# Kernel tuning notes

Measured on AMD Instinct MI355X. Metric: run time of the kernel, lower is better.

The kernel has to match this reference:

```python
import jax, jax.numpy as jnp
import numpy as np

D_MODEL = 512
NHEAD = 8
D_K = D_MODEL // NHEAD


def setup_inputs() -> dict:
    key = jax.random.key(0)
    ks = jax.random.split(key, 7)
    B, L = 4, 2048
    x = jax.random.normal(ks[0], (B, L, D_MODEL), dtype=jnp.float32)
    scale = 1.0 / np.sqrt(D_MODEL)
    Wq = jax.random.normal(ks[1], (D_MODEL, D_MODEL), dtype=jnp.float32) * scale
    Wk = jax.random.normal(ks[2], (D_MODEL, D_MODEL), dtype=jnp.float32) * scale
    Wv = jax.random.normal(ks[3], (D_MODEL, D_MODEL), dtype=jnp.float32) * scale
    Wo = jax.random.normal(ks[4], (D_MODEL, D_MODEL), dtype=jnp.float32) * scale
    wave_freq = jax.random.normal(ks[5], (NHEAD,), dtype=jnp.float32) * 0.1
    wave_phase = jnp.zeros((NHEAD,), dtype=jnp.float32)
    return {"x": x, "Wq": Wq, "Wk": Wk, "Wv": Wv, "Wo": Wo,
            "wave_freq": wave_freq, "wave_phase": wave_phase}


def reference(x, Wq, Wk, Wv, Wo, wave_freq, wave_phase):
    B, L, D = x.shape
    H, dk = NHEAD, D_K
    # nn.Linear(bias=False): y = x @ W.T
    q = (x @ Wq.T).reshape(B, L, H, dk).transpose(0, 2, 1, 3)  # (B,H,L,dk)
    k = (x @ Wk.T).reshape(B, L, H, dk).transpose(0, 2, 1, 3)
    v = (x @ Wv.T).reshape(B, L, H, dk).transpose(0, 2, 1, 3)
    pos = jnp.arange(L, dtype=x.dtype)  # (L,)
    two_pi = jnp.asarray(2.0 * np.pi, dtype=x.dtype)
    # wave: (H, L) -> broadcast as (1, H, 1, L) over key positions
    wave = jnp.cos(two_pi * wave_freq[:, None] * pos[None, :] + wave_phase[:, None])
    scores = jnp.einsum('bhqd,bhkd->bhqk', q, k) * (dk ** -0.5)
    scores = scores * wave[None, :, None, :]
    attn = jax.nn.softmax(scores, axis=-1)
    out = jnp.einsum('bhqk,bhkd->bhqd', attn, v)
    out = out.transpose(0, 2, 1, 3).reshape(B, L, D)
    return out @ Wo.T
```

## Files before the change

kernel.cpp:

```cpp
#include <hip/hip_runtime.h>
#include <math.h>

#define D_MODEL 512
#define NHEAD   8
#define DK      64
#define BATCH   4
#define SEQ     2048
#define MTOT    (BATCH*SEQ)
#define NXELEM  (MTOT*D_MODEL)
#define NWELEM  (4*D_MODEL*D_MODEL)

typedef _Float16 half8   __attribute__((ext_vector_type(8)));
typedef _Float16 half4_t __attribute__((ext_vector_type(4)));
typedef float    f32x4   __attribute__((ext_vector_type(4)));

#define MFMA32(a,b,c) __builtin_amdgcn_mfma_f32_16x16x32_f16((a),(b),(c),0,0,0)

__global__ __launch_bounds__(256) void cvt_kernel(
    const float* __restrict__ x,
    const float* __restrict__ Wq, const float* __restrict__ Wk,
    const float* __restrict__ Wv, const float* __restrict__ Wo,
    const float* __restrict__ wf, const float* __restrict__ wp,
    _Float16* __restrict__ Xh, _Float16* __restrict__ Wh,
    float* __restrict__ wtab)
{
    const int tid = blockIdx.x * 256 + threadIdx.x;
    int idx = tid * 4;
    if (idx < NXELEM + NWELEM) {
        const float* src; _Float16* dst; int off;
        if (idx < NXELEM) { src = x; dst = Xh; off = idx; }
        else {
            int r = idx - NXELEM;
            int sel = r >> 18;
            off = r & ((1 << 18) - 1);
            src = (sel == 0) ? Wq : (sel == 1) ? Wk : (sel == 2) ? Wv : Wo;
            dst = Wh + ((size_t)sel << 18);
        }
        float4 v = *(const float4*)(src + off);
        half4_t h;
        h[0] = (_Float16)v.x; h[1] = (_Float16)v.y;
        h[2] = (_Float16)v.z; h[3] = (_Float16)v.w;
        *(half4_t*)(dst + off) = h;
    } else {
        int widx = idx - (NXELEM + NWELEM);
        const int h = widx >> 11;
        const int pos0 = widx & 2047;
        const float f  = 6.28318530717958647692f * wf[h];
        const float ph = wp[h];
        float4 o;
        o.x = 0.125f * cosf(fmaf(f, (float)(pos0 + 0), ph));
        o.y = 0.125f * cosf(fmaf(f, (float)(pos0 + 1), ph));
        o.z = 0.125f * cosf(fmaf(f, (float)(pos0 + 2), ph));
        o.w = 0.125f * cosf(fmaf(f, (float)(pos0 + 3), ph));
        *(float4*)(wtab + widx) = o;
    }
}

__global__ __launch_bounds__(256) void qkv_mfma_kernel(
    const _Float16* __restrict__ Xh, const _Float16* __restrict__ Wh,
    const float* __restrict__ wtab,
    _Float16* __restrict__ Qh, _Float16* __restrict__ Kh,
    _Float16* __restrict__ Vth)
{
    __shared__ _Float16 As[128][72];
    __shared__ _Float16 Bs[64][72];

    const int t  = threadIdx.x;
    const int n0 = blockIdx.x * 64;
    const int m0 = blockIdx.y * 128;
    const int which = n0 >> 9;
    const int h = (n0 >> 6) & 7;
    const _Float16* Wbase = Wh + ((size_t)which << 18) + (size_t)(h * 64) * 512;

    const int w = t >> 6, lane = t & 63, ln = lane & 15, quad = lane >> 4;
    const int ar = t >> 1, ac = (t & 1) * 32;
    const int br = t >> 2, bc = (t & 3) * 16;

    const _Float16* ag = Xh + (size_t)(m0 + ar) * 512 + ac;
    const _Float16* bg = Wbase + (size_t)br * 512 + bc;

    const f32x4 kZero = {0.f, 0.f, 0.f, 0.f};
    f32x4 acc[2][4];
    #pragma unroll
    for (int i = 0; i < 2; ++i)
        #pragma unroll
        for (int j = 0; j < 4; ++j) acc[i][j] = kZero;

    for (int k0 = 0; k0 < 512; k0 += 64) {
        half8 av[4], bv[2];
        #pragma unroll
        for (int i = 0; i < 4; ++i) av[i] = *(const half8*)(ag + k0 + i * 8);
        #pragma unroll
        for (int i = 0; i < 2; ++i) bv[i] = *(const half8*)(bg + k0 + i * 8);
        __syncthreads();
        #pragma unroll
        for (int i = 0; i < 4; ++i) *(half8*)&As[ar][ac + i * 8] = av[i];
        #pragma unroll
        for (int i = 0; i < 2; ++i) *(half8*)&Bs[br][bc + i * 8] = bv[i];
        __syncthreads();

        #pragma unroll
        for (int ks = 0; ks < 2; ++ks) {
            half8 af[2], bf[4];
            #pragma unroll
            for (int mt = 0; mt < 2; ++mt)
                af[mt] = *(const half8*)&As[w * 32 + mt * 16 + ln][ks * 32 + quad * 8];
            #pragma unroll
            for (int nt = 0; nt < 4; ++nt)
                bf[nt] = *(const half8*)&Bs[nt * 16 + ln][ks * 32 + quad * 8];
            #pragma unroll
            for (int mt = 0; mt < 2; ++mt)
                #pragma unroll
                for (int nt = 0; nt < 4; ++nt)
                    acc[mt][nt] = MFMA32(af[mt], bf[nt], acc[mt][nt]);
        }
    }

    const int b  = m0 >> 11;
    const int l0 = m0 & 2047;

    if (which < 2) {
        _Float16* dst = (which == 0 ? Qh : Kh) + (size_t)(b * NHEAD + h) * SEQ * DK;
        const float* wt = wtab + h * SEQ;
        #pragma unroll
        for (int mt = 0; mt < 2; ++mt)
            #pragma unroll
            for (int r = 0; r < 4; ++r) {
                const int lq = l0 + w * 32 + mt * 16 + quad * 4 + r;
                const float wv = (which == 1) ? wt[lq] : 1.0f;
                #pragma unroll
                for (int nt = 0; nt < 4; ++nt) {
                    const int d = nt * 16 + ln;
                    dst[(size_t)lq * DK + d] = (_Float16)(acc[mt][nt][r] * wv);
                }
            }
    } else {
        __syncthreads();
        _Float16* Vl = &As[0][0];
        #pragma unroll
        for (int mt = 0; mt < 2; ++mt)
            #pragma unroll
            for (int nt = 0; nt < 4; ++nt)
                #pragma unroll
                for (int r = 0; r < 4; ++r) {
                    const int lq = w * 32 + mt * 16 + quad * 4 + r;
                    const int k32 = lq & 31;
                    const int pos = (lq & ~31) | (((k32 >> 2) & 3) << 3)
                                  | ((k32 >> 4) << 2) | (k32 & 3);
                    const int d  = nt * 16 + ln;
                    Vl[d * 136 + pos] = (_Float16)acc[mt][nt][r];
                }
        __syncthreads();
        _Float16* dst = Vth + (size_t)(b * NHEAD + h) * DK * SEQ;
        const int d = t >> 2, c0 = (t & 3) * 32;
        #pragma unroll
        for (int i = 0; i < 4; ++i) {
            half8 v = *(const half8*)&Vl[d * 136 + c0 + i * 8];
            *(half8*)(dst + (size_t)d * SEQ + l0 + c0 + i * 8) = v;
        }
    }
}

__global__ __launch_bounds__(256) void attn_mfma_kernel(
    const _Float16* __restrict__ Qh, const _Float16* __restrict__ Kwh,
    const _Float16* __restrict__ Vth, _Float16* __restrict__ AOh)
{
    __shared__ _Float16 Qs[64][72];
    __shared__ _Float16 Ks[64][72];
    __shared__ _Float16 Vs[64][72];

    const int bh = blockIdx.x;
    const int q0 = blockIdx.y * 64;
    const int b = bh >> 3, h = bh & 7;

    const int t = threadIdx.x;
    const int w = t >> 6, lane = t & 63, ln = lane & 15, quad = lane >> 4;

    const _Float16* Qg = Qh + ((size_t)bh * SEQ + q0) * DK;
    const _Float16* Kg = Kwh + (size_t)bh * SEQ * DK;
    const _Float16* Vg = Vth + (size_t)bh * DK * SEQ;

    const int sr = t >> 2, sc = (t & 3) * 16;

    *(half8*)&Qs[sr][sc]     = *(const half8*)(Qg + (size_t)sr * DK + sc);
    *(half8*)&Qs[sr][sc + 8] = *(const half8*)(Qg + (size_t)sr * DK + sc + 8);
    __syncthreads();
    half8 qf0 = *(const half8*)&Qs[w * 16 + ln][quad * 8];
    half8 qf1 = *(const half8*)&Qs[w * 16 + ln][32 + quad * 8];

    const f32x4 kZero = {0.f, 0.f, 0.f, 0.f};
    f32x4 o[4];
    #pragma unroll
    for (int nt = 0; nt < 4; ++nt) o[nt] = kZero;
    float l_acc = 0.f;

    for (int kt = 0; kt < SEQ; kt += 64) {
        half8 kv0 = *(const half8*)(Kg + (size_t)(kt + sr) * DK + sc);
        half8 kv1 = *(const half8*)(Kg + (size_t)(kt + sr) * DK + sc + 8);
        half8 vv0 = *(const half8*)(Vg + (size_t)sr * SEQ + kt + sc);
        half8 vv1 = *(const half8*)(Vg + (size_t)sr * SEQ + kt + sc + 8);
        __syncthreads();
        *(half8*)&Ks[sr][sc]     = kv0;
        *(half8*)&Ks[sr][sc + 8] = kv1;
        *(half8*)&Vs[sr][sc]     = vv0;
        *(half8*)&Vs[sr][sc + 8] = vv1;
        __syncthreads();

        #pragma unroll
        for (int g = 0; g < 2; ++g) {
            half8 ka0 = *(const half8*)&Ks[(2*g+0) * 16 + ln][quad * 8];
            half8 ka1 = *(const half8*)&Ks[(2*g+0) * 16 + ln][32 + quad * 8];
            half8 kb0 = *(const half8*)&Ks[(2*g+1) * 16 + ln][quad * 8];
            half8 kb1 = *(const half8*)&Ks[(2*g+1) * 16 + ln][32 + quad * 8];
            f32x4 s0 = MFMA32(ka0, qf0, kZero);
            f32x4 s1 = MFMA32(kb0, qf0, kZero);
            s0 = MFMA32(ka1, qf1, s0);
            s1 = MFMA32(kb1, qf1, s1);

            half8 pf;
            float ps = 0.f;
            #pragma unroll
            for (int r = 0; r < 4; ++r) {
                const float e0 = __expf(s0[r]);
                const float e1 = __expf(s1[r]);
                pf[r]     = (_Float16)e0;
                pf[r + 4] = (_Float16)e1;
                ps += e0 + e1;
            }
            l_acc += ps;

            #pragma unroll
            for (int nt = 0; nt < 4; ++nt) {
                half8 vf = *(const half8*)&Vs[nt * 16 + ln][g * 32 + quad * 8];
                o[nt] = MFMA32(pf, vf, o[nt]);
            }
        }
    }

    l_acc += __shfl_xor(l_acc, 16);
    l_acc += __shfl_xor(l_acc, 32);

    #pragma unroll
    for (int r = 0; r < 4; ++r) {
        const float lr  = __shfl(l_acc, quad * 4 + r, 16);
        const float inv = 1.0f / lr;
        const int lq = q0 + w * 16 + quad * 4 + r;
        const size_t base = ((size_t)b * SEQ + lq) * D_MODEL + h * DK;
        #pragma unroll
        for (int nt = 0; nt < 4; ++nt)
            AOh[base + nt * 16 + ln] = (_Float16)(o[nt][r] * inv);
    }
}

__global__ __launch_bounds__(256) void out_mfma_kernel(
    const _Float16* __restrict__ AOh, const _Float16* __restrict__ Woh,
    float* __restrict__ out)
{
    __shared__ _Float16 As[128][72];
    __shared__ _Float16 Bs[64][72];

    const int t  = threadIdx.x;
    const int n0 = blockIdx.x * 64;
    const int m0 = blockIdx.y * 128;

    const int w = t >> 6, lane = t & 63, ln = lane & 15, quad = lane >> 4;
    const int ar = t >> 1, ac = (t & 1) * 32;
    const int br = t >> 2, bc = (t & 3) * 16;

    const _Float16* ag = AOh + (size_t)(m0 + ar) * 512 + ac;
    const _Float16* bg = Woh + (size_t)(n0 + br) * 512 + bc;

    const f32x4 kZero = {0.f, 0.f, 0.f, 0.f};
    f32x4 acc[2][4];
    #pragma unroll
    for (int i = 0; i < 2; ++i)
        #pragma unroll
        for (int j = 0; j < 4; ++j) acc[i][j] = kZero;

    for (int k0 = 0; k0 < 512; k0 += 64) {
        half8 av[4], bv[2];
        #pragma unroll
        for (int i = 0; i < 4; ++i) av[i] = *(const half8*)(ag + k0 + i * 8);
        #pragma unroll
        for (int i = 0; i < 2; ++i) bv[i] = *(const half8*)(bg + k0 + i * 8);
        __syncthreads();
        #pragma unroll
        for (int i = 0; i < 4; ++i) *(half8*)&As[ar][ac + i * 8] = av[i];
        #pragma unroll
        for (int i = 0; i < 2; ++i) *(half8*)&Bs[br][bc + i * 8] = bv[i];
        __syncthreads();

        #pragma unroll
        for (int ks = 0; ks < 2; ++ks) {
            half8 af[2], bf[4];
            #pragma unroll
            for (int mt = 0; mt < 2; ++mt)
                af[mt] = *(const half8*)&As[w * 32 + mt * 16 + ln][ks * 32 + quad * 8];
            #pragma unroll
            for (int nt = 0; nt < 4; ++nt)
                bf[nt] = *(const half8*)&Bs[nt * 16 + ln][ks * 32 + quad * 8];
            #pragma unroll
            for (int mt = 0; mt < 2; ++mt)
                #pragma unroll
                for (int nt = 0; nt < 4; ++nt)
                    acc[mt][nt] = MFMA32(af[mt], bf[nt], acc[mt][nt]);
        }
    }

    #pragma unroll
    for (int mt = 0; mt < 2; ++mt)
        #pragma unroll
        for (int nt = 0; nt < 4; ++nt)
            #pragma unroll
            for (int r = 0; r < 4; ++r) {
                const int gm = m0 + w * 32 + mt * 16 + quad * 4 + r;
                out[(size_t)gm * 512 + n0 + nt * 16 + ln] = acc[mt][nt][r];
            }
}

extern "C" void kernel_launch(void* const* d_in, const int* in_sizes, int n_in,
                              void* d_out, int out_size, void* d_ws, size_t ws_size,
                              hipStream_t stream)
{
    (void)in_sizes; (void)n_in; (void)out_size; (void)ws_size;
    const float* x  = (const float*)d_in[0];
    const float* Wq = (const float*)d_in[1];
    const float* Wk = (const float*)d_in[2];
    const float* Wv = (const float*)d_in[3];
    const float* Wo = (const float*)d_in[4];
    const float* wf = (const float*)d_in[5];
    const float* wp = (const float*)d_in[6];
    float* out = (float*)d_out;

    const size_t NX = (size_t)MTOT * D_MODEL;
    _Float16* Xh  = (_Float16*)d_ws;
    _Float16* Wh  = Xh + NX;
    _Float16* Qh  = Wh + 4 * 262144;
    _Float16* Kh  = Qh + NX;
    _Float16* Vth = Kh + NX;
    _Float16* AOh = Vth + NX;
    float*    wtab = (float*)(AOh + NX);

    cvt_kernel<<<5136, 256, 0, stream>>>(x, Wq, Wk, Wv, Wo, wf, wp, Xh, Wh, wtab);

    dim3 g1(24, 64);
    qkv_mfma_kernel<<<g1, 256, 0, stream>>>(Xh, Wh, wtab, Qh, Kh, Vth);

    dim3 g2(BATCH * NHEAD, SEQ / 64);
    attn_mfma_kernel<<<g2, 256, 0, stream>>>(Qh, Kh, Vth, AOh);

    dim3 g3(8, 64);
    out_mfma_kernel<<<g3, 256, 0, stream>>>(AOh, Wh + 3 * 262144, out);
}
```

Measured before the change: 178.4 us.

## Double-buffer K/V tiles and process 128 queries per attention block

The attention kernel now covers 128 query rows per block, with two 16-row query tiles per wave, so each K/V tile loaded into shared memory is reused twice as often. K/V tiles are double-buffered and the next tile's global loads are issued before the current tile's compute. The grid is flattened to 512 blocks, with an index remap intended to place heads that share K/V close together. The cost is more accumulator registers and half as many blocks, which may lower occupancy and parallelism.

```diff
diff --git a/kernel.cpp b/kernel.cpp
--- a/kernel.cpp
+++ b/kernel.cpp
@@ -165,12 +165,13 @@
     const _Float16* __restrict__ Qh, const _Float16* __restrict__ Kwh,
     const _Float16* __restrict__ Vth, _Float16* __restrict__ AOh)
 {
-    __shared__ _Float16 Qs[64][72];
-    __shared__ _Float16 Ks[64][72];
-    __shared__ _Float16 Vs[64][72];
-
-    const int bh = blockIdx.x;
-    const int q0 = blockIdx.y * 64;
+    __shared__ _Float16 SM[4][64][72];
+
+    const int bx = blockIdx.x;
+    const int g8 = bx & 7;
+    const int s  = bx >> 3;
+    const int bh = g8 * 4 + (s >> 4);
+    const int q0 = (s & 15) * 128;
     const int b = bh >> 3, h = bh & 7;
 
     const int t = threadIdx.x;
@@ -181,75 +182,133 @@
     const _Float16* Vg = Vth + (size_t)bh * DK * SEQ;
 
     const int sr = t >> 2, sc = (t & 3) * 16;
-
-    *(half8*)&Qs[sr][sc]     = *(const half8*)(Qg + (size_t)sr * DK + sc);
-    *(half8*)&Qs[sr][sc + 8] = *(const half8*)(Qg + (size_t)sr * DK + sc + 8);
+    const int qr = t >> 1, qc = (t & 1) * 32;
+
+    {
+        const _Float16* qp = Qg + (size_t)qr * DK + qc;
+        half8 qv0 = *(const half8*)(qp);
+        half8 qv1 = *(const half8*)(qp + 8);
+        half8 qv2 = *(const half8*)(qp + 16);
+        half8 qv3 = *(const half8*)(qp + 24);
+        const _Float16* kp = Kg + (size_t)sr * DK + sc;
+        const _Float16* vp = Vg + (size_t)sr * SEQ + sc;
+        half8 kv0 = *(const half8*)(kp);
+        half8 kv1 = *(const half8*)(kp + 8);
+        half8 vv0 = *(const half8*)(vp);
+        half8 vv1 = *(const half8*)(vp + 8);
+        _Float16* qd = &SM[2 + (qr >> 6)][qr & 63][qc];
+        *(half8*)(qd)      = qv0;
+        *(half8*)(qd + 8)  = qv1;
+        *(half8*)(qd + 16) = qv2;
+        *(half8*)(qd + 24) = qv3;
+        *(half8*)&SM[0][sr][sc]     = kv0;
+        *(half8*)&SM[0][sr][sc + 8] = kv1;
+        *(half8*)&SM[1][sr][sc]     = vv0;
+        *(half8*)&SM[1][sr][sc + 8] = vv1;
+    }
     __syncthreads();
-    half8 qf0 = *(const half8*)&Qs[w * 16 + ln][quad * 8];
-    half8 qf1 = *(const half8*)&Qs[w * 16 + ln][32 + quad * 8];
+
+    half8 qf[2][2];
+    #pragma unroll
+    for (int u = 0; u < 2; ++u) {
+        const int row = w * 32 + u * 16 + ln;
+        const _Float16* qsrc = &SM[2 + (row >> 6)][row & 63][0];
+        qf[u][0] = *(const half8*)(qsrc + quad * 8);
+        qf[u][1] = *(const half8*)(qsrc + 32 + quad * 8);
+    }
+    __syncthreads();
 
     const f32x4 kZero = {0.f, 0.f, 0.f, 0.f};
-    f32x4 o[4];
-    #pragma unroll
-    for (int nt = 0; nt < 4; ++nt) o[nt] = kZero;
-    float l_acc = 0.f;
-
-    for (int kt = 0; kt < SEQ; kt += 64) {
-        half8 kv0 = *(const half8*)(Kg + (size_t)(kt + sr) * DK + sc);
-        half8 kv1 = *(const half8*)(Kg + (size_t)(kt + sr) * DK + sc + 8);
-        half8 vv0 = *(const half8*)(Vg + (size_t)sr * SEQ + kt + sc);
-        half8 vv1 = *(const half8*)(Vg + (size_t)sr * SEQ + kt + sc + 8);
-        __syncthreads();
-        *(half8*)&Ks[sr][sc]     = kv0;
-        *(half8*)&Ks[sr][sc + 8] = kv1;
-        *(half8*)&Vs[sr][sc]     = vv0;
-        *(half8*)&Vs[sr][sc + 8] = vv1;
-        __syncthreads();
+    f32x4 o[2][4];
+    #pragma unroll
+    for (int u = 0; u < 2; ++u)
+        #pragma unroll
+        for (int nt = 0; nt < 4; ++nt) o[u][nt] = kZero;
+    float l_acc[2] = {0.f, 0.f};
+
+    for (int kt = 0; kt < SEQ / 64; ++kt) {
+        const int cur = kt & 1;
+
+        half8 pk0, pk1, pv0, pv1;
+        const bool more = (kt + 1 < SEQ / 64);
+        if (more) {
+            const _Float16* kp = Kg + (size_t)((kt + 1) * 64 + sr) * DK + sc;
+            const _Float16* vp = Vg + (size_t)sr * SEQ + (kt + 1) * 64 + sc;
+            pk0 = *(const half8*)(kp);
+            pk1 = *(const half8*)(kp + 8);
+            pv0 = *(const half8*)(vp);
+            pv1 = *(const half8*)(vp + 8);
+        }
+
+        const _Float16 (*Ks)[72] = SM[2 * cur];
+        const _Float16 (*Vs)[72] = SM[2 * cur + 1];
 
         #pragma unroll
         for (int g = 0; g < 2; ++g) {
-            half8 ka0 = *(const half8*)&Ks[(2*g+0) * 16 + ln][quad * 8];
-            half8 ka1 = *(const half8*)&Ks[(2*g+0) * 16 + ln][32 + quad * 8];
-            half8 kb0 = *(const half8*)&Ks[(2*g+1) * 16 + ln][quad * 8];
-            half8 kb1 = *(const half8*)&Ks[(2*g+1) * 16 + ln][32 + quad * 8];
-            f32x4 s0 = MFMA32(ka0, qf0, kZero);
-            f32x4 s1 = MFMA32(kb0, qf0, kZero);
-            s0 = MFMA32(ka1, qf1, s0);
-            s1 = MFMA32(kb1, qf1, s1);
-
-            half8 pf;
-            float ps = 0.f;
-            #pragma unroll
-            for (int r = 0; r < 4; ++r) {
-                const float e0 = __expf(s0[r]);
-                const float e1 = __expf(s1[r]);
-                pf[r]     = (_Float16)e0;
-                pf[r + 4] = (_Float16)e1;
-                ps += e0 + e1;
+            half8 ka0 = *(const half8*)&Ks[(2 * g + 0) * 16 + ln][quad * 8];
+            half8 ka1 = *(const half8*)&Ks[(2 * g + 0) * 16 + ln][32 + quad * 8];
+            half8 kb0 = *(const half8*)&Ks[(2 * g + 1) * 16 + ln][quad * 8];
+            half8 kb1 = *(const half8*)&Ks[(2 * g + 1) * 16 + ln][32 + quad * 8];
+            half8 vf[4];
+            #pragma unroll
+            for (int nt = 0; nt < 4; ++nt)
+                vf[nt] = *(const half8*)&Vs[nt * 16 + ln][g * 32 + quad * 8];
+
+            #pragma unroll
+            for (int u = 0; u < 2; ++u) {
+                f32x4 s0 = MFMA32(ka0, qf[u][0], kZero);
+                f32x4 s1 = MFMA32(kb0, qf[u][0], kZero);
+                s0 = MFMA32(ka1, qf[u][1], s0);
+                s1 = MFMA32(kb1, qf[u][1], s1);
+
+                half8 pf;
+                float ps = 0.f;
+                #pragma unroll
+                for (int r = 0; r < 4; ++r) {
+                    const float e0 = __expf(s0[r]);
+                    const float e1 = __expf(s1[r]);
+                    pf[r]     = (_Float16)e0;
+                    pf[r + 4] = (_Float16)e1;
+                    ps += e0 + e1;
+                }
+                l_acc[u] += ps;
+
+                #pragma unroll
+                for (int nt = 0; nt < 4; ++nt)
+                    o[u][nt] = MFMA32(pf, vf[nt], o[u][nt]);
             }
-            l_acc += ps;
-
-            #pragma unroll
-            for (int nt = 0; nt < 4; ++nt) {
-                half8 vf = *(const half8*)&Vs[nt * 16 + ln][g * 32 + quad * 8];
-                o[nt] = MFMA32(pf, vf, o[nt]);
-            }
-        }
-    }
-
-    l_acc += __shfl_xor(l_acc, 16);
-    l_acc += __shfl_xor(l_acc, 32);
-
-    #pragma unroll
-    for (int r = 0; r < 4; ++r) {
-        const float lr  = __shfl(l_acc, quad * 4 + r, 16);
-        const float inv = 1.0f / lr;
-        const int lq = q0 + w * 16 + quad * 4 + r;
-        const size_t base = ((size_t)b * SEQ + lq) * D_MODEL + h * DK;
-        #pragma unroll
-        for (int nt = 0; nt < 4; ++nt)
-            AOh[base + nt * 16 + ln] = (_Float16)(o[nt][r] * inv);
-    }
+        }
+
+        __syncthreads();
+        if (more) {
+            _Float16* kd = &SM[2 * (cur ^ 1)][sr][sc];
+            _Float16* vd = &SM[2 * (cur ^ 1) + 1][sr][sc];
+            *(half8*)(kd)     = pk0;
+            *(half8*)(kd + 8) = pk1;
+            *(half8*)(vd)     = pv0;
+            *(half8*)(vd + 8) = pv1;
+        }
+        __syncthreads();
+    }
+
+    #pragma unroll
+    for (int u = 0; u < 2; ++u) {
+        l_acc[u] += __shfl_xor(l_acc[u], 16);
+        l_acc[u] += __shfl_xor(l_acc[u], 32);
+    }
+
+    #pragma unroll
+    for (int u = 0; u < 2; ++u)
+        #pragma unroll
+        for (int r = 0; r < 4; ++r) {
+            const float lr  = __shfl(l_acc[u], quad * 4 + r, 16);
+            const float inv = 1.0f / lr;
+            const int lq = q0 + w * 32 + u * 16 + quad * 4 + r;
+            const size_t base = ((size_t)b * SEQ + lq) * D_MODEL + h * DK;
+            #pragma unroll
+            for (int nt = 0; nt < 4; ++nt)
+                AOh[base + nt * 16 + ln] = (_Float16)(o[u][nt][r] * inv);
+        }
 }
 
 __global__ __launch_bounds__(256) void out_mfma_kernel(
@@ -346,8 +405,7 @@
     dim3 g1(24, 64);
     qkv_mfma_kernel<<<g1, 256, 0, stream>>>(Xh, Wh, wtab, Qh, Kh, Vth);
 
-    dim3 g2(BATCH * NHEAD, SEQ / 64);
-    attn_mfma_kernel<<<g2, 256, 0, stream>>>(Qh, Kh, Vth, AOh);
+    attn_mfma_kernel<<<512, 256, 0, stream>>>(Qh, Kh, Vth, AOh);
 
     dim3 g3(8, 64);
     out_mfma_kernel<<<g3, 256, 0, stream>>>(AOh, Wh + 3 * 262144, out);
```

After: 168.4 us. -5.6%, faster.
